# Kernel optimization log

Measured on AMD Instinct MI355X. Metric: run time of the kernel, lower is better.

## Reference

```python
import jax, jax.numpy as jnp
import numpy as np

B, S, D, NH, FF = 2, 2048, 1024, 16, 4096
HD = D // NH
SCALE = HD ** -0.5
EPS = 1e-5


def layer_norm(x, g, b):
    mu = jnp.mean(x, axis=-1, keepdims=True)
    var = jnp.var(x, axis=-1, keepdims=True)
    return (x - mu) * jax.lax.rsqrt(var + EPS) * g + b


def setup_inputs() -> dict:
    key = jax.random.key(0)
    ks = jax.random.split(key, 12)
    w = 0.02
    return {
        "x": jax.random.normal(ks[0], (B, S, D), dtype=jnp.float32),
        "ln1_g": jnp.ones((D,), jnp.float32),
        "ln1_b": jnp.zeros((D,), jnp.float32),
        "wq": jax.random.normal(ks[1], (D, D), jnp.float32) * w,
        "wkv": jax.random.normal(ks[2], (D, 2 * D), jnp.float32) * w,
        "wo": jax.random.normal(ks[3], (D, D), jnp.float32) * w,
        "bo": jnp.zeros((D,), jnp.float32),
        "ln2_g": jnp.ones((D,), jnp.float32),
        "ln2_b": jnp.zeros((D,), jnp.float32),
        "w1": jax.random.normal(ks[4], (D, FF), jnp.float32) * w,
        "b1": jnp.zeros((FF,), jnp.float32),
        "w2": jax.random.normal(ks[5], (FF, D), jnp.float32) * w,
        "b2": jnp.zeros((D,), jnp.float32),
    }


def reference(x, ln1_g, ln1_b, wq, wkv, wo, bo, ln2_g, ln2_b, w1, b1, w2, b2):
    # pre-norm self-attention (y=None -> keys = normalized queries), no mask
    h = layer_norm(x, ln1_g, ln1_b)                      # [B,S,D]
    q = (h @ wq).reshape(B, S, NH, HD)                   # [B,S,H,hd]
    kv = (h @ wkv).reshape(B, S, 2, NH, HD)
    k, v = kv[:, :, 0], kv[:, :, 1]                      # [B,S,H,hd]
    scores = jnp.einsum("bnhd,bmhd->bnmh", q, k) * SCALE  # [B,S,S,H]
    attn = jax.nn.softmax(scores, axis=2)
    o = jnp.einsum("bnmh,bmhd->bnhd", attn, v).reshape(B, S, D)
    o = o @ wo + bo
    x = x + o
    h2 = layer_norm(x, ln2_g, ln2_b)
    ff = jnp.maximum(h2 @ w1 + b1, 0.0) @ w2 + b2        # relu MLP, dropout p=0
    return (x + ff, attn)
```

## Files before the change

### kernel.cpp

```cpp
#include <hip/hip_runtime.h>
#include <hip/hip_bf16.h>


constexpr int Bc = 2, Sc = 2048, Dc = 1024, NHc = 16, FFc = 4096;
constexpr int Mrows = Bc * Sc;
constexpr float SCALE_ = 0.125f;
constexpr float EPSc = 1e-5f;
constexpr float L2E = 1.4426950408889634f;
constexpr float SC_L2E = SCALE_ * L2E;

typedef __attribute__((ext_vector_type(8))) short short8;
typedef __attribute__((ext_vector_type(4))) short short4v;
typedef __attribute__((ext_vector_type(4))) float floatx4;

#define DEV static __device__ __forceinline__

DEV short f2b(float f) {
  union { float f; unsigned u; } v; v.f = f;
  unsigned r = v.u + 0x7FFFu + ((v.u >> 16) & 1u);
  return (short)(r >> 16);
}

DEV floatx4 mfma16(short8 a, short8 b, floatx4 c) {
  return __builtin_amdgcn_mfma_f32_16x16x32_bf16(a, b, c, 0, 0, 0);
}

DEV void load_lds16(const short* g, short* l) {
  __builtin_amdgcn_global_load_lds(
      (const __attribute__((address_space(1))) void*)g,
      (__attribute__((address_space(3))) void*)l, 16, 0, 0);
}

__global__ __launch_bounds__(256) void cast_transpose_k(
    const float* __restrict__ W, short* __restrict__ Wt, int K, int N) {
  __shared__ float t[32][33];
  int n0 = blockIdx.x * 32, k0 = blockIdx.y * 32;
  int tx = threadIdx.x & 31, ty = threadIdx.x >> 5;
  for (int r = ty; r < 32; r += 8)
    t[r][tx] = W[(size_t)(k0 + r) * N + n0 + tx];
  __syncthreads();
  for (int r = ty; r < 32; r += 8)
    Wt[(size_t)(n0 + r) * K + k0 + tx] = f2b(t[tx][r]);
}

__global__ __launch_bounds__(256) void layernorm_k(
    const float* __restrict__ x, const float* __restrict__ g,
    const float* __restrict__ bb, short* __restrict__ out) {
  int row = blockIdx.x;
  float4 v = ((const float4*)(x + (size_t)row * Dc))[threadIdx.x];
  float s = v.x + v.y + v.z + v.w;
  float s2 = v.x * v.x + v.y * v.y + v.z * v.z + v.w * v.w;
#pragma unroll
  for (int off = 32; off >= 1; off >>= 1) {
    s += __shfl_xor(s, off);
    s2 += __shfl_xor(s2, off);
  }
  __shared__ float red[8];
  int wave = threadIdx.x >> 6, lane = threadIdx.x & 63;
  if (lane == 0) { red[wave] = s; red[4 + wave] = s2; }
  __syncthreads();
  s = red[0] + red[1] + red[2] + red[3];
  s2 = red[4] + red[5] + red[6] + red[7];
  float mu = s * (1.0f / Dc);
  float var = s2 * (1.0f / Dc) - mu * mu;
  float rstd = rsqrtf(var + EPSc);
  int c = threadIdx.x * 4;
  float4 gv = ((const float4*)g)[threadIdx.x];
  float4 bv = ((const float4*)bb)[threadIdx.x];
  short4v o;
  o.x = f2b((v.x - mu) * rstd * gv.x + bv.x);
  o.y = f2b((v.y - mu) * rstd * gv.y + bv.y);
  o.z = f2b((v.z - mu) * rstd * gv.z + bv.z);
  o.w = f2b((v.w - mu) * rstd * gv.w + bv.w);
  *(short4v*)(out + (size_t)row * Dc + c) = o;
}

template <int OUTF, int BN>
__global__ __launch_bounds__(256) void gemm_bt_k(
    const short* __restrict__ A, const short* __restrict__ Bt,
    const float* __restrict__ bias, const float* __restrict__ resid,
    void* __restrict__ Cout, int M, int N, int K, int relu) {
  constexpr int NJ = (BN == 128) ? 4 : 2;
  __shared__ short As[128 * 32];
  __shared__ short Bs[BN * 32];
  int tid = threadIdx.x;
  int wave = tid >> 6, lane = tid & 63, quad = lane >> 4, l16 = lane & 15;
  int m0 = blockIdx.y * 128, n0 = blockIdx.x * BN;
  int wm = (wave & 1) * 64;
  int wn = (wave >> 1) * (BN / 2);
  int lrow = lane >> 2, lcol = (lane & 3) * 8;
  const short* Ab0 = A + (size_t)(m0 + wave * 32 + lrow) * K + lcol;
  const short* Ab1 = A + (size_t)(m0 + wave * 32 + 16 + lrow) * K + lcol;
  short* Al0 = &As[(wave * 2 + 0) * 512];
  short* Al1 = &As[(wave * 2 + 1) * 512];
  const short* Bb0;
  const short* Bb1 = nullptr;
  short* Bl0;
  short* Bl1 = nullptr;
  if (BN == 128) {
    Bb0 = Bt + (size_t)(n0 + wave * 32 + lrow) * K + lcol;
    Bb1 = Bt + (size_t)(n0 + wave * 32 + 16 + lrow) * K + lcol;
    Bl0 = &Bs[(wave * 2 + 0) * 512];
    Bl1 = &Bs[(wave * 2 + 1) * 512];
  } else {
    Bb0 = Bt + (size_t)(n0 + wave * 16 + lrow) * K + lcol;
    Bl0 = &Bs[wave * 512];
  }
  floatx4 acc[4][NJ] = {};
  for (int k0 = 0; k0 < K; k0 += 32) {
    __syncthreads();
    load_lds16(Ab0 + k0, Al0);
    load_lds16(Ab1 + k0, Al1);
    load_lds16(Bb0 + k0, Bl0);
    if (BN == 128) load_lds16(Bb1 + k0, Bl1);
    __syncthreads();
    short8 af[4], bf[NJ];
#pragma unroll
    for (int i = 0; i < 4; ++i)
      af[i] = *(const short8*)(&As[(wm + i * 16 + l16) * 32 + quad * 8]);
#pragma unroll
    for (int j = 0; j < NJ; ++j)
      bf[j] = *(const short8*)(&Bs[(wn + j * 16 + l16) * 32 + quad * 8]);
#pragma unroll
    for (int i = 0; i < 4; ++i)
#pragma unroll
      for (int j = 0; j < NJ; ++j)
        acc[i][j] = mfma16(af[i], bf[j], acc[i][j]);
  }
#pragma unroll
  for (int i = 0; i < 4; ++i) {
    int row = m0 + wm + i * 16 + quad * 4;
#pragma unroll
    for (int j = 0; j < NJ; ++j) {
      int col = n0 + wn + j * 16 + l16;
      float bv = bias ? bias[col] : 0.0f;
#pragma unroll
      for (int r = 0; r < 4; ++r) {
        float v = acc[i][j][r] + bv;
        if (resid) v += resid[(size_t)(row + r) * N + col];
        if (relu) v = fmaxf(v, 0.0f);
        if (OUTF == 0)
          ((short*)Cout)[(size_t)(row + r) * N + col] = f2b(v);
        else
          ((float*)Cout)[(size_t)(row + r) * N + col] = v;
      }
    }
  }
}

__global__ __launch_bounds__(256) void transpose_v_k(
    const short* __restrict__ kv, short* __restrict__ vT) {
  __shared__ short t[64][65];
  int bh = blockIdx.y, b = bh >> 4, h = bh & 15;
  int m0 = blockIdx.x * 64;
  int c = threadIdx.x & 63, ty = threadIdx.x >> 6;
  for (int r = ty; r < 64; r += 4)
    t[r][c] = kv[(size_t)(b * Sc + m0 + r) * 2048 + 1024 + h * 64 + c];
  __syncthreads();
  for (int dd = ty; dd < 64; dd += 4)
    vT[((size_t)bh * 64 + dd) * Sc + m0 + c] = t[c][dd];
}

__global__ __launch_bounds__(256) void attn_stats_k(
    const short* __restrict__ q, const short* __restrict__ kv,
    float* __restrict__ m_i, float* __restrict__ inv_l) {
  int bh = blockIdx.y, b = bh >> 4, h = bh & 15;
  int wave = threadIdx.x >> 6, lane = threadIdx.x & 63, quad = lane >> 4,
      l16 = lane & 15;
  int n0 = blockIdx.x * 64 + wave * 16;
  const short* qp = q + (size_t)(b * Sc + n0 + l16) * Dc + h * 64 + quad * 8;
  short8 qf0 = *(const short8*)qp;
  short8 qf1 = *(const short8*)(qp + 32);
  const short* kb = kv + (size_t)b * Sc * 2048 + h * 64 + quad * 8;
  float rm[4], rl[4];
#pragma unroll
  for (int r = 0; r < 4; ++r) { rm[r] = -1e30f; rl[r] = 0.0f; }
  for (int m0 = 0; m0 < Sc; m0 += 16) {
    const short* kp = kb + (size_t)(m0 + l16) * 2048;
    short8 kf0 = *(const short8*)kp;
    short8 kf1 = *(const short8*)(kp + 32);
    floatx4 s = {0.0f, 0.0f, 0.0f, 0.0f};
    s = mfma16(qf0, kf0, s);
    s = mfma16(qf1, kf1, s);
#pragma unroll
    for (int r = 0; r < 4; ++r) {
      float sv = s[r] * SC_L2E;
      float nm = fmaxf(rm[r], sv);
      rl[r] = rl[r] * exp2f(rm[r] - nm) + exp2f(sv - nm);
      rm[r] = nm;
    }
  }
#pragma unroll
  for (int off = 1; off < 16; off <<= 1) {
#pragma unroll
    for (int r = 0; r < 4; ++r) {
      float om = __shfl_xor(rm[r], off);
      float ol = __shfl_xor(rl[r], off);
      float nm = fmaxf(rm[r], om);
      rl[r] = rl[r] * exp2f(rm[r] - nm) + ol * exp2f(om - nm);
      rm[r] = nm;
    }
  }
  if (l16 == 0) {
    int n = n0 + quad * 4;
#pragma unroll
    for (int r = 0; r < 4; ++r) {
      m_i[(size_t)bh * Sc + n + r] = rm[r];
      inv_l[(size_t)bh * Sc + n + r] = 1.0f / rl[r];
    }
  }
}

__global__ __launch_bounds__(256) void attn_fused_k(
    const short* __restrict__ q, const short* __restrict__ kv,
    const short* __restrict__ vT, const float* __restrict__ m_i,
    const float* __restrict__ inv_l, float* __restrict__ attn,
    float* __restrict__ opart) {
  constexpr int HP = 20;
  __shared__ float P[16 * 32 * HP];
  __shared__ short pw[4][16 * 40];
  __shared__ float sm[16][16], sl[16][16];
  int b = blockIdx.z, mc = blockIdx.x;
  int n0 = blockIdx.y * 16;
  int tid = threadIdx.x;
  int wave = tid >> 6, lane = tid & 63, quad = lane >> 4, l16 = lane & 15;
  {
    int h = tid >> 4, nn = tid & 15;
    sm[h][nn] = m_i[(size_t)(b * 16 + h) * Sc + n0 + nn];
    sl[h][nn] = inv_l[(size_t)(b * 16 + h) * Sc + n0 + nn];
  }
  short8 qf[4][2];
#pragma unroll
  for (int hh = 0; hh < 4; ++hh) {
    const short* qp =
        q + (size_t)(b * Sc + n0 + l16) * Dc + (wave * 4 + hh) * 64 + quad * 8;
    qf[hh][0] = *(const short8*)qp;
    qf[hh][1] = *(const short8*)(qp + 32);
  }
  floatx4 oacc[4][4] = {};
  short* myP = &pw[wave][0];
  __syncthreads();
  int mend = mc * 512 + 512;
  for (int m0 = mc * 512; m0 < mend; m0 += 32) {
#pragma unroll
    for (int hh = 0; hh < 4; ++hh) {
      int h = wave * 4 + hh;
      const short* kb =
          kv + (size_t)(b * Sc + m0 + l16) * 2048 + h * 64 + quad * 8;
#pragma unroll
      for (int ms = 0; ms < 2; ++ms) {
        const short* kp = kb + (size_t)ms * 16 * 2048;
        short8 kf0 = *(const short8*)kp;
        short8 kf1 = *(const short8*)(kp + 32);
        floatx4 s = {0.0f, 0.0f, 0.0f, 0.0f};
        s = mfma16(qf[hh][0], kf0, s);
        s = mfma16(qf[hh][1], kf1, s);
#pragma unroll
        for (int r = 0; r < 4; ++r) {
          int nn = quad * 4 + r;
          float p = exp2f(s[r] * SC_L2E - sm[h][nn]) * sl[h][nn];
          P[(nn * 32 + ms * 16 + l16) * HP + h] = p;
          myP[nn * 40 + ms * 16 + l16] = f2b(p);
        }
      }
      short8 pa = *(const short8*)(&myP[l16 * 40 + quad * 8]);
      const short* vb = vT + ((size_t)(b * 16 + h) * 64) * Sc;
#pragma unroll
      for (int dt = 0; dt < 4; ++dt) {
        short8 vf =
            *(const short8*)(vb + (size_t)(dt * 16 + l16) * Sc + m0 + quad * 8);
        oacc[hh][dt] = mfma16(pa, vf, oacc[hh][dt]);
      }
    }
    __syncthreads();
    size_t base = (((size_t)b * Sc + n0) * Sc + m0) * 16;
    for (int t = tid; t < 2048; t += 256) {
      int nn = t >> 7, rem = t & 127;
      int ml = rem >> 2, h4 = (rem & 3) * 4;
      float4 v = *(const float4*)&P[(nn * 32 + ml) * HP + h4];
      *(float4*)&attn[base + (size_t)nn * (Sc * 16) + ml * 16 + h4] = v;
    }
    __syncthreads();
  }
  float* op = opart + (size_t)mc * ((size_t)Bc * Sc * Dc) +
              ((size_t)b * Sc + n0) * Dc;
#pragma unroll
  for (int hh = 0; hh < 4; ++hh)
#pragma unroll
    for (int dt = 0; dt < 4; ++dt)
#pragma unroll
      for (int r = 0; r < 4; ++r)
        op[(size_t)(quad * 4 + r) * Dc + (wave * 4 + hh) * 64 + dt * 16 + l16] =
            oacc[hh][dt][r];
}

__global__ __launch_bounds__(256) void opart_reduce_k(
    const float* __restrict__ op, short* __restrict__ o) {
  const size_t PS = (size_t)Bc * Sc * Dc;
  const size_t n4 = PS / 4;
  for (size_t i = (size_t)blockIdx.x * 256 + threadIdx.x; i < n4;
       i += (size_t)gridDim.x * 256) {
    float4 a = ((const float4*)op)[i];
    float4 b = ((const float4*)(op + PS))[i];
    float4 c = ((const float4*)(op + 2 * PS))[i];
    float4 d = ((const float4*)(op + 3 * PS))[i];
    short4v s;
    s.x = f2b(a.x + b.x + c.x + d.x);
    s.y = f2b(a.y + b.y + c.y + d.y);
    s.z = f2b(a.z + b.z + c.z + d.z);
    s.w = f2b(a.w + b.w + c.w + d.w);
    ((short4v*)o)[i] = s;
  }
}

extern "C" void kernel_launch(void* const* d_in, const int* in_sizes, int n_in,
                              void* d_out, int out_size, void* d_ws,
                              size_t ws_size, hipStream_t stream) {
  const float* x = (const float*)d_in[0];
  const float* ln1g = (const float*)d_in[1];
  const float* ln1b = (const float*)d_in[2];
  const float* wq = (const float*)d_in[3];
  const float* wkv = (const float*)d_in[4];
  const float* wo = (const float*)d_in[5];
  const float* bo = (const float*)d_in[6];
  const float* ln2g = (const float*)d_in[7];
  const float* ln2b = (const float*)d_in[8];
  const float* w1 = (const float*)d_in[9];
  const float* b1 = (const float*)d_in[10];
  const float* w2 = (const float*)d_in[11];
  const float* b2 = (const float*)d_in[12];

  char* ws = (char*)d_ws;
  const size_t MB = 1024 * 1024;
  short* wqT  = (short*)(ws + 0 * MB);
  short* wkvT = (short*)(ws + 2 * MB);
  short* woT  = (short*)(ws + 6 * MB);
  short* w1T  = (short*)(ws + 8 * MB);
  short* w2T  = (short*)(ws + 16 * MB);
  short* h    = (short*)(ws + 24 * MB);
  float* x2   = (float*)(ws + 32 * MB);
  float* m_i  = (float*)(ws + 48 * MB);
  float* invl = (float*)(ws + 48 * MB + 256 * 1024);
  short* o    = (short*)(ws + 49 * MB);
  short* qb   = (short*)(ws + 57 * MB);
  short* kvb  = (short*)(ws + 65 * MB);
  short* vT   = (short*)(ws + 81 * MB);
  float* opart= (float*)(ws + 96 * MB);
  short* ff1  = (short*)(ws + 57 * MB);

  float* out0 = (float*)d_out;
  float* attn = (float*)d_out + (size_t)Bc * Sc * Dc;

  cast_transpose_k<<<dim3(Dc / 32, Dc / 32), 256, 0, stream>>>(wq, wqT, Dc, Dc);
  cast_transpose_k<<<dim3(2048 / 32, Dc / 32), 256, 0, stream>>>(wkv, wkvT, Dc, 2048);
  cast_transpose_k<<<dim3(Dc / 32, Dc / 32), 256, 0, stream>>>(wo, woT, Dc, Dc);
  cast_transpose_k<<<dim3(FFc / 32, Dc / 32), 256, 0, stream>>>(w1, w1T, Dc, FFc);
  cast_transpose_k<<<dim3(Dc / 32, FFc / 32), 256, 0, stream>>>(w2, w2T, FFc, Dc);

  layernorm_k<<<Mrows, 256, 0, stream>>>(x, ln1g, ln1b, h);

  gemm_bt_k<0, 64><<<dim3(Dc / 64, Mrows / 128), 256, 0, stream>>>(
      h, wqT, nullptr, nullptr, qb, Mrows, Dc, Dc, 0);
  gemm_bt_k<0, 128><<<dim3(2048 / 128, Mrows / 128), 256, 0, stream>>>(
      h, wkvT, nullptr, nullptr, kvb, Mrows, 2048, Dc, 0);

  transpose_v_k<<<dim3(Sc / 64, Bc * NHc), 256, 0, stream>>>(kvb, vT);
  attn_stats_k<<<dim3(Sc / 64, Bc * NHc), 256, 0, stream>>>(qb, kvb, m_i, invl);
  attn_fused_k<<<dim3(4, Sc / 16, Bc), 256, 0, stream>>>(
      qb, kvb, vT, m_i, invl, attn, opart);
  opart_reduce_k<<<2048, 256, 0, stream>>>(opart, o);

  gemm_bt_k<1, 64><<<dim3(Dc / 64, Mrows / 128), 256, 0, stream>>>(
      o, woT, bo, x, x2, Mrows, Dc, Dc, 0);
  layernorm_k<<<Mrows, 256, 0, stream>>>(x2, ln2g, ln2b, h);
  gemm_bt_k<0, 128><<<dim3(FFc / 128, Mrows / 128), 256, 0, stream>>>(
      h, w1T, b1, nullptr, ff1, Mrows, FFc, Dc, 1);
  gemm_bt_k<1, 64><<<dim3(Dc / 64, Mrows / 128), 256, 0, stream>>>(
      ff1, w2T, b2, x2, out0, Mrows, Dc, FFc, 0);
}
```

Measured before the change: 1.225 ms.

## Merge weight casts, fuse V transpose into KV GEMM, remap attention grids

All five weight cast-transpose launches become one kernel that picks its matrix from the flat block index. The KV projection GEMM now writes the V half straight into the transposed vT layout from its accumulators, so the separate transpose_v kernel and its extra pass over kvb go away. The attention stats and fused kernels switch to 1D grids with a swizzled block-to-(batch, head, chunk) mapping, apparently to improve cache locality across concurrently running blocks. The fused V store writes 4-element column pieces strided by Sc, which may coalesce worse than the old LDS transpose, and the V half of kvb is no longer written.

```diff
diff --git a/kernel.cpp b/kernel.cpp
--- a/kernel.cpp
+++ b/kernel.cpp
@@ -31,10 +31,21 @@
       (__attribute__((address_space(3))) void*)l, 16, 0, 0);
 }
 
-__global__ __launch_bounds__(256) void cast_transpose_k(
-    const float* __restrict__ W, short* __restrict__ Wt, int K, int N) {
+__global__ __launch_bounds__(256) void cast_transpose_all_k(
+    const float* __restrict__ wq, const float* __restrict__ wkv,
+    const float* __restrict__ wo, const float* __restrict__ w1,
+    const float* __restrict__ w2, short* __restrict__ wqT,
+    short* __restrict__ wkvT, short* __restrict__ woT,
+    short* __restrict__ w1T, short* __restrict__ w2T) {
   __shared__ float t[32][33];
-  int n0 = blockIdx.x * 32, k0 = blockIdx.y * 32;
+  int bid = blockIdx.x;
+  const float* W; short* Wt; int K, N, bx, by;
+  if (bid < 1024)      { W = wq;  Wt = wqT;  K = 1024; N = 1024; int u = bid;        bx = u & 31;  by = u >> 5; }
+  else if (bid < 3072) { W = wkv; Wt = wkvT; K = 1024; N = 2048; int u = bid - 1024; bx = u & 63;  by = u >> 6; }
+  else if (bid < 4096) { W = wo;  Wt = woT;  K = 1024; N = 1024; int u = bid - 3072; bx = u & 31;  by = u >> 5; }
+  else if (bid < 8192) { W = w1;  Wt = w1T;  K = 1024; N = 4096; int u = bid - 4096; bx = u & 127; by = u >> 7; }
+  else                 { W = w2;  Wt = w2T;  K = 4096; N = 1024; int u = bid - 8192; bx = u & 31;  by = u >> 5; }
+  int n0 = bx * 32, k0 = by * 32;
   int tx = threadIdx.x & 31, ty = threadIdx.x >> 5;
   for (int r = ty; r < 32; r += 8)
     t[r][tx] = W[(size_t)(k0 + r) * N + n0 + tx];
@@ -79,7 +90,8 @@
 __global__ __launch_bounds__(256) void gemm_bt_k(
     const short* __restrict__ A, const short* __restrict__ Bt,
     const float* __restrict__ bias, const float* __restrict__ resid,
-    void* __restrict__ Cout, int M, int N, int K, int relu) {
+    void* __restrict__ Cout, int M, int N, int K, int relu,
+    short* __restrict__ vTout) {
   constexpr int NJ = (BN == 128) ? 4 : 2;
   __shared__ short As[128 * 32];
   __shared__ short Bs[BN * 32];
@@ -127,6 +139,26 @@
       for (int j = 0; j < NJ; ++j)
         acc[i][j] = mfma16(af[i], bf[j], acc[i][j]);
   }
+  if (vTout != nullptr && n0 >= 1024) {
+#pragma unroll
+    for (int i = 0; i < 4; ++i) {
+      int row = m0 + wm + i * 16 + quad * 4;
+      int bb = row >> 11, mloc = row & 2047;
+#pragma unroll
+      for (int j = 0; j < NJ; ++j) {
+        int dg = n0 + wn + j * 16 + l16 - 1024;
+        short4v pk;
+        pk.x = f2b(acc[i][j][0]);
+        pk.y = f2b(acc[i][j][1]);
+        pk.z = f2b(acc[i][j][2]);
+        pk.w = f2b(acc[i][j][3]);
+        *(short4v*)(vTout +
+                    ((size_t)(bb * 16 + (dg >> 6)) * 64 + (dg & 63)) * Sc +
+                    mloc) = pk;
+      }
+    }
+    return;
+  }
 #pragma unroll
   for (int i = 0; i < 4; ++i) {
     int row = m0 + wm + i * 16 + quad * 4;
@@ -148,26 +180,17 @@
   }
 }
 
-__global__ __launch_bounds__(256) void transpose_v_k(
-    const short* __restrict__ kv, short* __restrict__ vT) {
-  __shared__ short t[64][65];
-  int bh = blockIdx.y, b = bh >> 4, h = bh & 15;
-  int m0 = blockIdx.x * 64;
-  int c = threadIdx.x & 63, ty = threadIdx.x >> 6;
-  for (int r = ty; r < 64; r += 4)
-    t[r][c] = kv[(size_t)(b * Sc + m0 + r) * 2048 + 1024 + h * 64 + c];
-  __syncthreads();
-  for (int dd = ty; dd < 64; dd += 4)
-    vT[((size_t)bh * 64 + dd) * Sc + m0 + c] = t[c][dd];
-}
-
 __global__ __launch_bounds__(256) void attn_stats_k(
     const short* __restrict__ q, const short* __restrict__ kv,
     float* __restrict__ m_i, float* __restrict__ inv_l) {
-  int bh = blockIdx.y, b = bh >> 4, h = bh & 15;
+  int bid = blockIdx.x;
+  int r_ = bid >> 3;
+  int bh = (bid & 7) * 4 + (r_ >> 5);
+  int nb = r_ & 31;
+  int b = bh >> 4, h = bh & 15;
   int wave = threadIdx.x >> 6, lane = threadIdx.x & 63, quad = lane >> 4,
       l16 = lane & 15;
-  int n0 = blockIdx.x * 64 + wave * 16;
+  int n0 = nb * 64 + wave * 16;
   const short* qp = q + (size_t)(b * Sc + n0 + l16) * Dc + h * 64 + quad * 8;
   short8 qf0 = *(const short8*)qp;
   short8 qf1 = *(const short8*)(qp + 32);
@@ -220,8 +243,10 @@
   __shared__ float P[16 * 32 * HP];
   __shared__ short pw[4][16 * 40];
   __shared__ float sm[16][16], sl[16][16];
-  int b = blockIdx.z, mc = blockIdx.x;
-  int n0 = blockIdx.y * 16;
+  int bid = blockIdx.x;
+  int g = bid & 7;
+  int b = g >> 2, mc = g & 3;
+  int n0 = (bid >> 3) * 16;
   int tid = threadIdx.x;
   int wave = tid >> 6, lane = tid & 63, quad = lane >> 4, l16 = lane & 15;
   {
@@ -351,30 +376,25 @@
   float* out0 = (float*)d_out;
   float* attn = (float*)d_out + (size_t)Bc * Sc * Dc;
 
-  cast_transpose_k<<<dim3(Dc / 32, Dc / 32), 256, 0, stream>>>(wq, wqT, Dc, Dc);
-  cast_transpose_k<<<dim3(2048 / 32, Dc / 32), 256, 0, stream>>>(wkv, wkvT, Dc, 2048);
-  cast_transpose_k<<<dim3(Dc / 32, Dc / 32), 256, 0, stream>>>(wo, woT, Dc, Dc);
-  cast_transpose_k<<<dim3(FFc / 32, Dc / 32), 256, 0, stream>>>(w1, w1T, Dc, FFc);
-  cast_transpose_k<<<dim3(Dc / 32, FFc / 32), 256, 0, stream>>>(w2, w2T, FFc, Dc);
+  cast_transpose_all_k<<<12288, 256, 0, stream>>>(
+      wq, wkv, wo, w1, w2, wqT, wkvT, woT, w1T, w2T);
 
   layernorm_k<<<Mrows, 256, 0, stream>>>(x, ln1g, ln1b, h);
 
   gemm_bt_k<0, 64><<<dim3(Dc / 64, Mrows / 128), 256, 0, stream>>>(
-      h, wqT, nullptr, nullptr, qb, Mrows, Dc, Dc, 0);
+      h, wqT, nullptr, nullptr, qb, Mrows, Dc, Dc, 0, nullptr);
   gemm_bt_k<0, 128><<<dim3(2048 / 128, Mrows / 128), 256, 0, stream>>>(
-      h, wkvT, nullptr, nullptr, kvb, Mrows, 2048, Dc, 0);
-
-  transpose_v_k<<<dim3(Sc / 64, Bc * NHc), 256, 0, stream>>>(kvb, vT);
-  attn_stats_k<<<dim3(Sc / 64, Bc * NHc), 256, 0, stream>>>(qb, kvb, m_i, invl);
-  attn_fused_k<<<dim3(4, Sc / 16, Bc), 256, 0, stream>>>(
-      qb, kvb, vT, m_i, invl, attn, opart);
+      h, wkvT, nullptr, nullptr, kvb, Mrows, 2048, Dc, 0, vT);
+
+  attn_stats_k<<<1024, 256, 0, stream>>>(qb, kvb, m_i, invl);
+  attn_fused_k<<<1024, 256, 0, stream>>>(qb, kvb, vT, m_i, invl, attn, opart);
   opart_reduce_k<<<2048, 256, 0, stream>>>(opart, o);
 
   gemm_bt_k<1, 64><<<dim3(Dc / 64, Mrows / 128), 256, 0, stream>>>(
-      o, woT, bo, x, x2, Mrows, Dc, Dc, 0);
+      o, woT, bo, x, x2, Mrows, Dc, Dc, 0, nullptr);
   layernorm_k<<<Mrows, 256, 0, stream>>>(x2, ln2g, ln2b, h);
   gemm_bt_k<0, 128><<<dim3(FFc / 128, Mrows / 128), 256, 0, stream>>>(
-      h, w1T, b1, nullptr, ff1, Mrows, FFc, Dc, 1);
+      h, w1T, b1, nullptr, ff1, Mrows, FFc, Dc, 1, nullptr);
   gemm_bt_k<1, 64><<<dim3(Dc / 64, Mrows / 128), 256, 0, stream>>>(
-      ff1, w2T, b2, x2, out0, Mrows, Dc, FFc, 0);
-}
+      ff1, w2T, b2, x2, out0, Mrows, Dc, FFc, 0, nullptr);
+}
```

New measurement: 1.195 ms. -2.5%, faster.
